# Kernel optimization log

Measured on AMD Instinct MI355X. Metric: run time of the kernel, lower is better.

## Reference

```python
import jax, jax.numpy as jnp
import numpy as np

B, N, D = 8, 256, 128


def setup_inputs() -> dict:
    key = jax.random.key(0)
    ks = jax.random.split(key, 4)
    s1 = 1.0 / np.sqrt(4 * D)
    s2 = 1.0 / np.sqrt(2 * D)
    s3 = 1.0 / np.sqrt(D)
    return {
        "tour_features": jax.random.normal(ks[0], (B, N, D), dtype=jnp.float32),
        "W1": jax.random.uniform(ks[1], (4 * D, 2 * D), jnp.float32, -s1, s1),
        "b1": jnp.zeros((2 * D,), jnp.float32),
        "W2": jax.random.uniform(ks[2], (2 * D, D), jnp.float32, -s2, s2),
        "b2": jnp.zeros((D,), jnp.float32),
        "W3": jax.random.uniform(ks[3], (D, 1), jnp.float32, -s3, s3),
        "b3": jnp.zeros((1,), jnp.float32),
    }


def reference(tour_features, W1, b1, W2, b2, W3, b3):
    Bs, Ns, Ds = tour_features.shape
    x = tour_features
    x_next = jnp.roll(x, -1, axis=1)  # node at (k+1) % N
    # Split first linear's weight by the 4 concatenated feature blocks:
    # cat([x_i, x_{i+1}, x_j, x_{j+1}]) @ W1 == x_i@W1a + x_{i+1}@W1b + x_j@W1c + x_{j+1}@W1d
    W1a, W1b, W1c, W1d = jnp.split(W1, 4, axis=0)
    Pi = x @ W1a + x_next @ W1b          # [B, N, 2D] (i-side projection)
    Pj = x @ W1c + x_next @ W1d          # [B, N, 2D] (j-side projection)
    h1 = jax.nn.relu(Pi[:, :, None, :] + Pj[:, None, :, :] + b1)  # [B, N, N, 2D]
    h2 = jax.nn.relu(h1 @ W2 + b2)       # [B, N, N, D]
    score = jnp.tanh((h2 @ W3 + b3)[..., 0])  # [B, N, N]
    # Valid pairs: j >= i + 2 and not (j - i == N - 1)
    ii = jnp.arange(Ns)[:, None]
    jj = jnp.arange(Ns)[None, :]
    mask = (jj >= ii + 2) & (jj - ii != Ns - 1)
    improvement_matrix = jnp.where(mask[None], score, 0.0)
    improved_tour = jnp.broadcast_to(jnp.arange(Ns), (Bs, Ns))
    return improved_tour, improvement_matrix
```

## Files before the change

kernel.cpp:

```cpp
#include <hip/hip_runtime.h>


typedef __attribute__((ext_vector_type(8))) short short8;
typedef __attribute__((ext_vector_type(8))) _Float16 half8;
typedef __attribute__((ext_vector_type(4))) float floatx4;

static __device__ __forceinline__ unsigned short f2bf(float f) {
  unsigned int x = __float_as_uint(f);
  x += 0x7fff + ((x >> 16) & 1);
  return (unsigned short)(x >> 16);
}

static __device__ __forceinline__ unsigned short f2h(float f) {
  _Float16 h = (_Float16)f;
  return __builtin_bit_cast(unsigned short, h);
}

static __device__ __forceinline__ float fast_tanh(float x) {
  float e = __expf(2.0f * fabsf(x));
  float t = 1.0f - 2.0f * __builtin_amdgcn_rcpf(e + 1.0f);
  return copysignf(t, x);
}

static __device__ __forceinline__ long pack_fp8(half8 s) {
  int lo = __builtin_amdgcn_cvt_pk_fp8_f32((float)s[0], (float)s[1], 0, false);
  lo = __builtin_amdgcn_cvt_pk_fp8_f32((float)s[2], (float)s[3], lo, true);
  int hi = __builtin_amdgcn_cvt_pk_fp8_f32((float)s[4], (float)s[5], 0, false);
  hi = __builtin_amdgcn_cvt_pk_fp8_f32((float)s[6], (float)s[7], hi, true);
  return (long)(unsigned)lo | ((long)hi << 32);
}

__global__ __launch_bounds__(256) void k_prep(
    const float* __restrict__ x, const float* __restrict__ W1,
    const float* __restrict__ W2, float* __restrict__ out,
    unsigned char* __restrict__ W2F8, unsigned short* __restrict__ W1T,
    unsigned short* __restrict__ xcat) {
  int e = blockIdx.x * 256 + threadIdx.x;
  if (e < 2048) {
    out[e] = (float)(e & 255);
  } else if (e < 526336) {
    out[e] = 0.f;
  } else if (e < 542720) {
    int t = e - 526336;
    int p = t >> 7, n = t & 127;
    float f0 = W2[(2 * p) * 128 + n] * 16.f;
    float f1 = W2[(2 * p + 1) * 128 + n] * 16.f;
    int v = __builtin_amdgcn_cvt_pk_fp8_f32(f0, f1, 0, false);
    *(unsigned short*)(W2F8 + n * 256 + 2 * p) = (unsigned short)(v & 0xffff);
  } else if (e < 673792) {
    int e3 = e - 542720;
    int n = e3 >> 8, k = e3 & 255;
    W1T[e3] = f2bf(W1[((k + (n & 256)) << 8) + (n & 255)]);
  } else {
    int e4 = e - 673792;
    int r = e4 >> 8, k = e4 & 255;
    int pos = r & 255;
    int pos2 = (k < 128) ? pos : ((pos + 1) & 255);
    xcat[e4] = f2bf(x[(((r >> 8) << 8) + pos2) * 128 + (k & 127)]);
  }
}

__global__ __launch_bounds__(256) void k_proj(
    const unsigned short* __restrict__ xcat, const unsigned short* __restrict__ W1T,
    const float* __restrict__ b1, unsigned short* __restrict__ PiH,
    unsigned short* __restrict__ PjH) {
  const int mg = blockIdx.x >> 3;
  const int ng = blockIdx.x & 7;
  const int tid = threadIdx.x;
  const int wr = tid >> 6, lane = tid & 63, quad = lane >> 4, l15 = lane & 15;

  __shared__ unsigned short As[64 * 256];
  __shared__ unsigned short Bs[64 * 256];

#pragma unroll
  for (int it = 0; it < 8; ++it) {
    int e = it * 256 + tid;
    int r = e >> 5, v = e & 31;
    int col = ((v & 16) | ((v ^ (r & 15)) & 15)) << 3;
    *(uint4*)&As[r * 256 + col] = *(const uint4*)(xcat + (mg * 64 + r) * 256 + v * 8);
    *(uint4*)&Bs[r * 256 + col] = *(const uint4*)(W1T + (ng * 64 + r) * 256 + v * 8);
  }
  __syncthreads();

  floatx4 acc[4];
#pragma unroll
  for (int mt = 0; mt < 4; ++mt) acc[mt] = (floatx4)0.f;

  const char* Ab = (const char*)As;
  const char* Bb = (const char*)Bs + wr * 16 * 512;
  const int base_sw = l15 * 512 + ((quad ^ l15) << 4);

#pragma unroll
  for (int ks = 0; ks < 8; ++ks) {
    const int swz = base_sw ^ (ks << 6);
    short8 bfr = *(const short8*)(Bb + swz);
#pragma unroll
    for (int mt = 0; mt < 4; ++mt) {
      short8 afr = *(const short8*)(Ab + mt * 8192 + swz);
      acc[mt] = __builtin_amdgcn_mfma_f32_16x16x32_bf16(afr, bfr, acc[mt], 0, 0, 0);
    }
  }

  const int ch = ng * 64 + wr * 16 + l15;
  const float bias = (ch < 256) ? b1[ch] : 0.f;
  unsigned short* dst = (ch < 256) ? PiH : PjH;
  const int chan = ch & 255;
#pragma unroll
  for (int mt = 0; mt < 4; ++mt)
#pragma unroll
    for (int r = 0; r < 4; ++r) {
      int row = mg * 64 + mt * 16 + quad * 4 + r;
      dst[row * 256 + chan] = f2h(acc[mt][r] + bias);
    }
}

__global__ __launch_bounds__(256, 3) void k_main(
    const unsigned short* __restrict__ PiH, const unsigned short* __restrict__ PjH,
    const unsigned char* __restrict__ W2F8, const float* __restrict__ b2,
    const float* __restrict__ W3, const float* __restrict__ b3,
    float* __restrict__ outm) {
  const int tid = threadIdx.x;
  const int wr = tid >> 6;
  const int lane = tid & 63, quad = lane >> 4, l15 = lane & 15;

  __shared__ unsigned char W2s[128 * 256];

#pragma unroll
  for (int it = 0; it < 8; ++it) {
    int e = it * 256 + tid;
    int n = e >> 4, v = e & 15;
    *(uint4*)&W2s[n * 256 + ((v ^ (n & 15)) << 4)] =
        *(const uint4*)(W2F8 + n * 256 + v * 16);
  }
  __syncthreads();

  const int e2 = blockIdx.x * 4 + wr;
  const int b = (int)(((unsigned)e2 * 14769u) >> 24);
  const int e = e2 - b * 1136;
  int jt = 0, base = 0;
  if (e >= 30)  { jt = 1; base = 30;  }
  if (e >= 92)  { jt = 2; base = 92;  }
  if (e >= 186) { jt = 3; base = 186; }
  if (e >= 312) { jt = 4; base = 312; }
  if (e >= 470) { jt = 5; base = 470; }
  if (e >= 660) { jt = 6; base = 660; }
  if (e >= 882) { jt = 7; base = 882; }
  const int i = e - base;

  const char* W2base = (const char*)&W2s[0];
  const int base_sw = l15 * 256 + ((((quad >> 1) ^ l15) & 15) << 4) + ((quad & 1) << 3);
  const unsigned short* Pjb = PjH + ((b << 8) + jt * 32 + l15) * 256 + quad * 8;
  const unsigned short* PiRow = PiH + ((b << 8) + i) * 256 + quad * 8;

  floatx4 acc[2][8];
#pragma unroll
  for (int mt = 0; mt < 2; ++mt)
#pragma unroll
    for (int nt = 0; nt < 8; ++nt) acc[mt][nt] = (floatx4)0.f;

  union U4 { uint4 v; half8 h; };
  U4 piR[2], pjR[2][2];
  piR[0].v = *(const uint4*)(PiRow);
  pjR[0][0].v = *(const uint4*)(Pjb);
  pjR[0][1].v = *(const uint4*)(Pjb + 4096);

#pragma unroll
  for (int ks = 0; ks < 8; ++ks) {
    const int cur = ks & 1, nxt = cur ^ 1;
    long bfr[8];
    const char* baddr = W2base + (base_sw ^ (ks << 5));
#pragma unroll
    for (int nt = 0; nt < 8; ++nt) bfr[nt] = *(const long*)(baddr + nt * 4096);
    if (ks < 7) {
      piR[nxt].v = *(const uint4*)(PiRow + (ks + 1) * 32);
      pjR[nxt][0].v = *(const uint4*)(Pjb + (ks + 1) * 32);
      pjR[nxt][1].v = *(const uint4*)(Pjb + 4096 + (ks + 1) * 32);
    }
    const half8 s0 = __builtin_elementwise_max(piR[cur].h + pjR[cur][0].h,
                                               (half8)(_Float16)0);
    const half8 s1 = __builtin_elementwise_max(piR[cur].h + pjR[cur][1].h,
                                               (half8)(_Float16)0);
    const long a0 = pack_fp8(s0);
    const long a1 = pack_fp8(s1);
#pragma unroll
    for (int nt = 0; nt < 8; ++nt) {
      acc[0][nt] = __builtin_amdgcn_mfma_f32_16x16x32_fp8_fp8(a0, bfr[nt], acc[0][nt], 0, 0, 0);
      acc[1][nt] = __builtin_amdgcn_mfma_f32_16x16x32_fp8_fp8(a1, bfr[nt], acc[1][nt], 0, 0, 0);
    }
  }

  float* orow = outm + ((b << 8) + i) * 256 + jt * 32;
  const float b3v = b3[0];
  const float s16 = 0.0625f;
#pragma unroll
  for (int mt = 0; mt < 2; ++mt) {
    float p0 = 0, p1 = 0, p2 = 0, p3 = 0;
#pragma unroll
    for (int nt = 0; nt < 8; ++nt) {
      float w3v = W3[nt * 16 + l15];
      float b2v = b2[nt * 16 + l15];
      floatx4 a = acc[mt][nt];
      p0 += fmaxf(fmaf(a[0], s16, b2v), 0.f) * w3v;
      p1 += fmaxf(fmaf(a[1], s16, b2v), 0.f) * w3v;
      p2 += fmaxf(fmaf(a[2], s16, b2v), 0.f) * w3v;
      p3 += fmaxf(fmaf(a[3], s16, b2v), 0.f) * w3v;
    }
#pragma unroll
    for (int m = 8; m >= 1; m >>= 1) {
      p0 += __shfl_xor(p0, m, 16);
      p1 += __shfl_xor(p1, m, 16);
      p2 += __shfl_xor(p2, m, 16);
      p3 += __shfl_xor(p3, m, 16);
    }
    if (l15 == 0) {
      const int jl = jt * 32 + mt * 16 + quad * 4;
      float ps[4] = {p0, p1, p2, p3};
#pragma unroll
      for (int r = 0; r < 4; ++r) {
        int j = jl + r;
        float sc = fast_tanh(ps[r] + b3v);
        bool valid = (j >= i + 2) && (j - i != 255);
        orow[mt * 16 + quad * 4 + r] = valid ? sc : 0.f;
      }
    }
  }
}

extern "C" void kernel_launch(void* const* d_in, const int* in_sizes, int n_in,
                              void* d_out, int out_size, void* d_ws, size_t ws_size,
                              hipStream_t stream) {
  const float* x  = (const float*)d_in[0];
  const float* W1 = (const float*)d_in[1];
  const float* b1 = (const float*)d_in[2];
  const float* W2 = (const float*)d_in[3];
  const float* b2 = (const float*)d_in[4];
  const float* W3 = (const float*)d_in[5];
  const float* b3 = (const float*)d_in[6];
  float* out = (float*)d_out;

  unsigned short* PiH  = (unsigned short*)d_ws;
  unsigned short* PjH  = PiH + 524288;
  unsigned short* W1T  = PjH + 524288;
  unsigned short* xcat = W1T + 131072;
  unsigned char*  W2F8 = (unsigned char*)(xcat + 524288);

  k_prep<<<4680, 256, 0, stream>>>(x, W1, W2, out, W2F8, W1T, xcat);
  k_proj<<<256, 256, 0, stream>>>(xcat, W1T, b1, PiH, PjH);
  k_main<<<2272, 256, 0, stream>>>(PiH, PjH, W2F8, b2, W3, b3, out + 2048);
}
```

Before: 103.5 us.

## Pre-swizzle operands, use direct global-to-LDS loads, persistent k_main

The prep kernel now writes W1T, xcat and the fp8 W2 already in the swizzled LDS layout. This lets k_proj and k_main stage them with global_load_lds DMA instead of going through registers. k_main becomes a persistent grid of 1024 blocks, each wave looping over work items, which amortises the W2 LDS fill; occupancy goes to 4 waves per SIMD. The B-fragment loads are split into two halves interleaved with the MFMAs, with s_setprio raised around the MFMA bursts. Risks are load imbalance in the strided persistent loop (9088 items over 4096 waves) and register pressure under the tighter launch bound.

Result: slower. 161.5 us (+56.1%).

```diff
diff --git a/kernel.cpp b/kernel.cpp
--- a/kernel.cpp
+++ b/kernel.cpp
@@ -28,6 +28,12 @@
   int hi = __builtin_amdgcn_cvt_pk_fp8_f32((float)s[4], (float)s[5], 0, false);
   hi = __builtin_amdgcn_cvt_pk_fp8_f32((float)s[6], (float)s[7], hi, true);
   return (long)(unsigned)lo | ((long)hi << 32);
+}
+
+static __device__ __forceinline__ void gload_lds16(const void* g, void* l) {
+  __builtin_amdgcn_global_load_lds(
+      (const __attribute__((address_space(1))) unsigned int*)g,
+      (__attribute__((address_space(3))) unsigned int*)l, 16, 0, 0);
 }
 
 __global__ __launch_bounds__(256) void k_prep(
@@ -45,18 +51,24 @@
     int p = t >> 7, n = t & 127;
     float f0 = W2[(2 * p) * 128 + n] * 16.f;
     float f1 = W2[(2 * p + 1) * 128 + n] * 16.f;
-    int v = __builtin_amdgcn_cvt_pk_fp8_f32(f0, f1, 0, false);
-    *(unsigned short*)(W2F8 + n * 256 + 2 * p) = (unsigned short)(v & 0xffff);
+    int v2 = __builtin_amdgcn_cvt_pk_fp8_f32(f0, f1, 0, false);
+    int col = 2 * p;
+    int sw = (((col >> 4) ^ (n & 15)) << 4) | (col & 15);
+    *(unsigned short*)(W2F8 + n * 256 + sw) = (unsigned short)(v2 & 0xffff);
   } else if (e < 673792) {
     int e3 = e - 542720;
     int n = e3 >> 8, k = e3 & 255;
-    W1T[e3] = f2bf(W1[((k + (n & 256)) << 8) + (n & 255)]);
+    int v = k >> 3;
+    int sw = (((v & 16) | ((v ^ (n & 15)) & 15)) << 3) | (k & 7);
+    W1T[(n << 8) + sw] = f2bf(W1[((k + (n & 256)) << 8) + (n & 255)]);
   } else {
     int e4 = e - 673792;
     int r = e4 >> 8, k = e4 & 255;
+    int v = k >> 3;
+    int sw = (((v & 16) | ((v ^ (r & 15)) & 15)) << 3) | (k & 7);
     int pos = r & 255;
     int pos2 = (k < 128) ? pos : ((pos + 1) & 255);
-    xcat[e4] = f2bf(x[(((r >> 8) << 8) + pos2) * 128 + (k & 127)]);
+    xcat[(r << 8) + sw] = f2bf(x[(((r >> 8) << 8) + pos2) * 128 + (k & 127)]);
   }
 }
 
@@ -72,13 +84,13 @@
   __shared__ unsigned short As[64 * 256];
   __shared__ unsigned short Bs[64 * 256];
 
+  const unsigned short* Asrc = xcat + mg * 64 * 256;
+  const unsigned short* Bsrc = W1T + ng * 64 * 256;
 #pragma unroll
   for (int it = 0; it < 8; ++it) {
-    int e = it * 256 + tid;
-    int r = e >> 5, v = e & 31;
-    int col = ((v & 16) | ((v ^ (r & 15)) & 15)) << 3;
-    *(uint4*)&As[r * 256 + col] = *(const uint4*)(xcat + (mg * 64 + r) * 256 + v * 8);
-    *(uint4*)&Bs[r * 256 + col] = *(const uint4*)(W1T + (ng * 64 + r) * 256 + v * 8);
+    const int c = it * 256 + wr * 64 + lane;
+    gload_lds16(Asrc + c * 8, &As[(it * 256 + wr * 64) * 8]);
+    gload_lds16(Bsrc + c * 8, &Bs[(it * 256 + wr * 64) * 8]);
   }
   __syncthreads();
 
@@ -114,7 +126,7 @@
     }
 }
 
-__global__ __launch_bounds__(256, 3) void k_main(
+__global__ __launch_bounds__(256, 4) void k_main(
     const unsigned short* __restrict__ PiH, const unsigned short* __restrict__ PjH,
     const unsigned char* __restrict__ W2F8, const float* __restrict__ b2,
     const float* __restrict__ W3, const float* __restrict__ b3,
@@ -127,100 +139,113 @@
 
 #pragma unroll
   for (int it = 0; it < 8; ++it) {
-    int e = it * 256 + tid;
-    int n = e >> 4, v = e & 15;
-    *(uint4*)&W2s[n * 256 + ((v ^ (n & 15)) << 4)] =
-        *(const uint4*)(W2F8 + n * 256 + v * 16);
+    const int c = it * 256 + wr * 64 + lane;
+    gload_lds16(W2F8 + c * 16, &W2s[(it * 256 + wr * 64) * 16]);
   }
   __syncthreads();
-
-  const int e2 = blockIdx.x * 4 + wr;
-  const int b = (int)(((unsigned)e2 * 14769u) >> 24);
-  const int e = e2 - b * 1136;
-  int jt = 0, base = 0;
-  if (e >= 30)  { jt = 1; base = 30;  }
-  if (e >= 92)  { jt = 2; base = 92;  }
-  if (e >= 186) { jt = 3; base = 186; }
-  if (e >= 312) { jt = 4; base = 312; }
-  if (e >= 470) { jt = 5; base = 470; }
-  if (e >= 660) { jt = 6; base = 660; }
-  if (e >= 882) { jt = 7; base = 882; }
-  const int i = e - base;
 
   const char* W2base = (const char*)&W2s[0];
   const int base_sw = l15 * 256 + ((((quad >> 1) ^ l15) & 15) << 4) + ((quad & 1) << 3);
-  const unsigned short* Pjb = PjH + ((b << 8) + jt * 32 + l15) * 256 + quad * 8;
-  const unsigned short* PiRow = PiH + ((b << 8) + i) * 256 + quad * 8;
-
-  floatx4 acc[2][8];
-#pragma unroll
-  for (int mt = 0; mt < 2; ++mt)
-#pragma unroll
-    for (int nt = 0; nt < 8; ++nt) acc[mt][nt] = (floatx4)0.f;
-
-  union U4 { uint4 v; half8 h; };
-  U4 piR[2], pjR[2][2];
-  piR[0].v = *(const uint4*)(PiRow);
-  pjR[0][0].v = *(const uint4*)(Pjb);
-  pjR[0][1].v = *(const uint4*)(Pjb + 4096);
-
-#pragma unroll
-  for (int ks = 0; ks < 8; ++ks) {
-    const int cur = ks & 1, nxt = cur ^ 1;
-    long bfr[8];
-    const char* baddr = W2base + (base_sw ^ (ks << 5));
-#pragma unroll
-    for (int nt = 0; nt < 8; ++nt) bfr[nt] = *(const long*)(baddr + nt * 4096);
-    if (ks < 7) {
-      piR[nxt].v = *(const uint4*)(PiRow + (ks + 1) * 32);
-      pjR[nxt][0].v = *(const uint4*)(Pjb + (ks + 1) * 32);
-      pjR[nxt][1].v = *(const uint4*)(Pjb + 4096 + (ks + 1) * 32);
-    }
-    const half8 s0 = __builtin_elementwise_max(piR[cur].h + pjR[cur][0].h,
-                                               (half8)(_Float16)0);
-    const half8 s1 = __builtin_elementwise_max(piR[cur].h + pjR[cur][1].h,
-                                               (half8)(_Float16)0);
-    const long a0 = pack_fp8(s0);
-    const long a1 = pack_fp8(s1);
-#pragma unroll
-    for (int nt = 0; nt < 8; ++nt) {
-      acc[0][nt] = __builtin_amdgcn_mfma_f32_16x16x32_fp8_fp8(a0, bfr[nt], acc[0][nt], 0, 0, 0);
-      acc[1][nt] = __builtin_amdgcn_mfma_f32_16x16x32_fp8_fp8(a1, bfr[nt], acc[1][nt], 0, 0, 0);
-    }
-  }
-
-  float* orow = outm + ((b << 8) + i) * 256 + jt * 32;
   const float b3v = b3[0];
   const float s16 = 0.0625f;
-#pragma unroll
-  for (int mt = 0; mt < 2; ++mt) {
-    float p0 = 0, p1 = 0, p2 = 0, p3 = 0;
-#pragma unroll
-    for (int nt = 0; nt < 8; ++nt) {
-      float w3v = W3[nt * 16 + l15];
-      float b2v = b2[nt * 16 + l15];
-      floatx4 a = acc[mt][nt];
-      p0 += fmaxf(fmaf(a[0], s16, b2v), 0.f) * w3v;
-      p1 += fmaxf(fmaf(a[1], s16, b2v), 0.f) * w3v;
-      p2 += fmaxf(fmaf(a[2], s16, b2v), 0.f) * w3v;
-      p3 += fmaxf(fmaf(a[3], s16, b2v), 0.f) * w3v;
-    }
-#pragma unroll
-    for (int m = 8; m >= 1; m >>= 1) {
-      p0 += __shfl_xor(p0, m, 16);
-      p1 += __shfl_xor(p1, m, 16);
-      p2 += __shfl_xor(p2, m, 16);
-      p3 += __shfl_xor(p3, m, 16);
-    }
-    if (l15 == 0) {
-      const int jl = jt * 32 + mt * 16 + quad * 4;
-      float ps[4] = {p0, p1, p2, p3};
-#pragma unroll
-      for (int r = 0; r < 4; ++r) {
-        int j = jl + r;
-        float sc = fast_tanh(ps[r] + b3v);
-        bool valid = (j >= i + 2) && (j - i != 255);
-        orow[mt * 16 + quad * 4 + r] = valid ? sc : 0.f;
+
+#pragma unroll 1
+  for (int e2 = blockIdx.x * 4 + wr; e2 < 9088; e2 += 4096) {
+    const int b = (int)(((unsigned)e2 * 14769u) >> 24);
+    const int e = e2 - b * 1136;
+    int jt = 0, base = 0;
+    if (e >= 30)  { jt = 1; base = 30;  }
+    if (e >= 92)  { jt = 2; base = 92;  }
+    if (e >= 186) { jt = 3; base = 186; }
+    if (e >= 312) { jt = 4; base = 312; }
+    if (e >= 470) { jt = 5; base = 470; }
+    if (e >= 660) { jt = 6; base = 660; }
+    if (e >= 882) { jt = 7; base = 882; }
+    const int i = e - base;
+
+    const unsigned short* Pjb = PjH + ((b << 8) + jt * 32 + l15) * 256 + quad * 8;
+    const unsigned short* PiRow = PiH + ((b << 8) + i) * 256 + quad * 8;
+
+    floatx4 acc[2][8];
+#pragma unroll
+    for (int mt = 0; mt < 2; ++mt)
+#pragma unroll
+      for (int nt = 0; nt < 8; ++nt) acc[mt][nt] = (floatx4)0.f;
+
+    union U4 { uint4 v; half8 h; };
+    U4 piR[2], pjR[2][2];
+    piR[0].v = *(const uint4*)(PiRow);
+    pjR[0][0].v = *(const uint4*)(Pjb);
+    pjR[0][1].v = *(const uint4*)(Pjb + 4096);
+
+#pragma unroll
+    for (int ks = 0; ks < 8; ++ks) {
+      const int cur = ks & 1, nxt = cur ^ 1;
+      if (ks < 7) {
+        piR[nxt].v = *(const uint4*)(PiRow + (ks + 1) * 32);
+        pjR[nxt][0].v = *(const uint4*)(Pjb + (ks + 1) * 32);
+        pjR[nxt][1].v = *(const uint4*)(Pjb + 4096 + (ks + 1) * 32);
+      }
+      const char* baddr = W2base + (base_sw ^ (ks << 5));
+      long bfr0[4];
+#pragma unroll
+      for (int nt = 0; nt < 4; ++nt) bfr0[nt] = *(const long*)(baddr + nt * 4096);
+      const half8 s0 = __builtin_elementwise_max(piR[cur].h + pjR[cur][0].h,
+                                                 (half8)(_Float16)0);
+      const half8 s1 = __builtin_elementwise_max(piR[cur].h + pjR[cur][1].h,
+                                                 (half8)(_Float16)0);
+      const long a0 = pack_fp8(s0);
+      const long a1 = pack_fp8(s1);
+      __builtin_amdgcn_s_setprio(1);
+#pragma unroll
+      for (int nt = 0; nt < 4; ++nt) {
+        acc[0][nt] = __builtin_amdgcn_mfma_f32_16x16x32_fp8_fp8(a0, bfr0[nt], acc[0][nt], 0, 0, 0);
+        acc[1][nt] = __builtin_amdgcn_mfma_f32_16x16x32_fp8_fp8(a1, bfr0[nt], acc[1][nt], 0, 0, 0);
+      }
+      __builtin_amdgcn_s_setprio(0);
+      long bfr1[4];
+#pragma unroll
+      for (int nt = 0; nt < 4; ++nt) bfr1[nt] = *(const long*)(baddr + (nt + 4) * 4096);
+      __builtin_amdgcn_s_setprio(1);
+#pragma unroll
+      for (int nt = 0; nt < 4; ++nt) {
+        acc[0][nt + 4] = __builtin_amdgcn_mfma_f32_16x16x32_fp8_fp8(a0, bfr1[nt], acc[0][nt + 4], 0, 0, 0);
+        acc[1][nt + 4] = __builtin_amdgcn_mfma_f32_16x16x32_fp8_fp8(a1, bfr1[nt], acc[1][nt + 4], 0, 0, 0);
+      }
+      __builtin_amdgcn_s_setprio(0);
+    }
+
+    float* orow = outm + ((b << 8) + i) * 256 + jt * 32;
+#pragma unroll
+    for (int mt = 0; mt < 2; ++mt) {
+      float p0 = 0, p1 = 0, p2 = 0, p3 = 0;
+#pragma unroll
+      for (int nt = 0; nt < 8; ++nt) {
+        float w3v = W3[nt * 16 + l15];
+        float b2v = b2[nt * 16 + l15];
+        floatx4 a = acc[mt][nt];
+        p0 += fmaxf(fmaf(a[0], s16, b2v), 0.f) * w3v;
+        p1 += fmaxf(fmaf(a[1], s16, b2v), 0.f) * w3v;
+        p2 += fmaxf(fmaf(a[2], s16, b2v), 0.f) * w3v;
+        p3 += fmaxf(fmaf(a[3], s16, b2v), 0.f) * w3v;
+      }
+#pragma unroll
+      for (int m = 8; m >= 1; m >>= 1) {
+        p0 += __shfl_xor(p0, m, 16);
+        p1 += __shfl_xor(p1, m, 16);
+        p2 += __shfl_xor(p2, m, 16);
+        p3 += __shfl_xor(p3, m, 16);
+      }
+      if (l15 == 0) {
+        const int jl = jt * 32 + mt * 16 + quad * 4;
+        float ps[4] = {p0, p1, p2, p3};
+#pragma unroll
+        for (int r = 0; r < 4; ++r) {
+          int j = jl + r;
+          float sc = fast_tanh(ps[r] + b3v);
+          bool valid = (j >= i + 2) && (j - i != 255);
+          orow[mt * 16 + quad * 4 + r] = valid ? sc : 0.f;
+        }
       }
     }
   }
@@ -246,5 +271,5 @@
 
   k_prep<<<4680, 256, 0, stream>>>(x, W1, W2, out, W2F8, W1T, xcat);
   k_proj<<<256, 256, 0, stream>>>(xcat, W1T, b1, PiH, PjH);
-  k_main<<<2272, 256, 0, stream>>>(PiH, PjH, W2F8, b2, W3, b3, out + 2048);
-}
+  k_main<<<1024, 256, 0, stream>>>(PiH, PjH, W2F8, b2, W3, b3, out + 2048);
+}
```
